# Kernel tuning notes

Hardware: AMD Instinct MI355X
Metric: run time of the kernel (lower is better)

The kernel has to match this reference:

```python
import jax, jax.numpy as jnp
import numpy as np

B, T, N, D = 64, 12, 207, 128
H, ORDER = 8, 2
HID = 2 * D  # mlp_ratio = 2


def _ln(x, g, b, eps=1e-5):
    m = x.mean(-1, keepdims=True)
    v = ((x - m) ** 2).mean(-1, keepdims=True)
    return (x - m) * jax.lax.rsqrt(v + eps) * g + b


def _l2norm(t, eps=1e-12):
    # matches torch.nn.functional.normalize(dim=-1)
    n = jnp.sqrt((t * t).sum(-1, keepdims=True))
    return t / jnp.maximum(n, eps)


def _fast_attn(q, k, v):
    # q, k, v: (B2, L, H, Dh); Performer-style linear attention from FastAttentionLayer.fast_attention
    q = _l2norm(q)
    k = _l2norm(k)
    L = q.shape[1]
    kvs = jnp.einsum('blhm,blhd->bhmd', k, v)
    num = jnp.einsum('bnhm,bhmd->bnhd', q, kvs) + L * v
    ks_sum = k.sum(axis=1)  # (B2, H, Dh)
    den = jnp.einsum('bnhm,bhm->bnh', q, ks_sum)[..., None] + L
    return num / jnp.maximum(den, 1e-5)


def _fast_layer(x, qkv_w, out_w, out_b):
    # x: (B, T, N, D). qkv_bias=False (mask arg), kernel=3 -> out_proj: Linear(2D, D)
    b, t, n, d = x.shape
    dh = d // H
    qkv = x @ qkv_w.T  # (B, T, N, 3D)
    q, k, v = jnp.split(qkv, 3, axis=-1)
    # spatial pass: attend over the N nodes for each (b, t)
    out_s = _fast_attn(q.reshape(b * t, n, H, dh),
                       k.reshape(b * t, n, H, dh),
                       v.reshape(b * t, n, H, dh)).reshape(b, t, n, d)
    # temporal pass: attend over the T steps for each (b, n)
    qt = q.transpose(0, 2, 1, 3).reshape(b * n, t, H, dh)
    kt = k.transpose(0, 2, 1, 3).reshape(b * n, t, H, dh)
    vt = v.transpose(0, 2, 1, 3).reshape(b * n, t, H, dh)
    out_t = _fast_attn(qt, kt, vt).reshape(b, n, t, d).transpose(0, 2, 1, 3)
    return jnp.concatenate([out_s, out_t], -1) @ out_w.T + out_b


def _forward(x, graph, qkv_w, out_w, out_b, pw_w, pw_b,
             fc1_w, fc1_b, fc2_w, fc2_b, ln1_g, ln1_b, ln2_g, ln2_b):
    # GraphPropagate: x_list = [x, graph @ x, ...] (Ks = ORDER hops)
    xs = [x]
    xk = x
    for _ in range(ORDER - 1):
        xk = jnp.einsum('thi,btij->bthj', graph, xk)
        xs.append(xk)
    # per-hop fast attention + zero-init pointwise branch, summed over hops
    agg = jnp.zeros_like(x)
    for i in range(ORDER):
        agg = agg + _fast_layer(xs[i], qkv_w[i], out_w[i], out_b[i]) + xs[i] @ pw_w[i].T + pw_b[i]
    h = _ln(x + agg, ln1_g, ln1_b)
    ff = jax.nn.relu(h @ fc1_w.T + fc1_b) @ fc2_w.T + fc2_b
    return _ln(h + ff, ln2_g, ln2_b)


def setup_inputs() -> dict:
    key = jax.random.key(0)
    ks = jax.random.split(key, 8)
    s = 0.02
    return {
        'x': jax.random.normal(ks[0], (B, T, N, D), jnp.float32),
        'graph': jax.random.uniform(ks[1], (T, N, N), jnp.float32) / N,
        'qkv_w': jax.random.normal(ks[2], (ORDER, 3 * D, D), jnp.float32) * s,
        'out_w': jax.random.normal(ks[3], (ORDER, D, 2 * D), jnp.float32) * s,
        'out_b': jnp.zeros((ORDER, D), jnp.float32),
        'pw_w': jax.random.normal(ks[4], (ORDER, D, D), jnp.float32) * s,
        'pw_b': jnp.zeros((ORDER, D), jnp.float32),
        'fc1_w': jax.random.normal(ks[5], (HID, D), jnp.float32) * s,
        'fc1_b': jnp.zeros((HID,), jnp.float32),
        'fc2_w': jax.random.normal(ks[6], (D, HID), jnp.float32) * s,
        'fc2_b': jnp.zeros((D,), jnp.float32),
        'ln1_g': jnp.ones((D,), jnp.float32),
        'ln1_b': jnp.zeros((D,), jnp.float32),
        'ln2_g': jnp.ones((D,), jnp.float32),
        'ln2_b': jnp.zeros((D,), jnp.float32),
    }


def reference(x, graph, qkv_w, out_w, out_b, pw_w, pw_b,
              fc1_w, fc1_b, fc2_w, fc2_b, ln1_g, ln1_b, ln2_g, ln2_b):
    return _forward(x, graph, qkv_w, out_w, out_b, pw_w, pw_b,
                    fc1_w, fc1_b, fc2_w, fc2_b, ln1_g, ln1_b, ln2_g, ln2_b)
```

## Files before the change

kernel.cpp:

```cpp
#include <hip/hip_runtime.h>
#include <hip/hip_bf16.h>

#define BB 64
#define TT 12
#define NN 207
#define DD 128
#define HH 8
#define DH 16
#define MROWS (BB*TT*NN)
#define KPAD 224
#define AW 768
#define CHB 32
#define CROWS (CHB*TT*NN)

typedef __bf16 bf16x8 __attribute__((ext_vector_type(8)));
typedef float  f32x4  __attribute__((ext_vector_type(4)));

__device__ inline float  b2f(__bf16 v){ return (float)v; }
__device__ inline __bf16 f2b(float v){ return (__bf16)v; }
__device__ inline bf16x8 ldfrag(const __bf16* p){ return *reinterpret_cast<const bf16x8*>(p); }

__device__ inline void gload_lds16(const __bf16* g, __bf16* l){
    __builtin_amdgcn_global_load_lds(
        (const __attribute__((address_space(1))) void*)(g),
        (__attribute__((address_space(3))) void*)(l), 16, 0, 0);
}
__device__ inline int swz(int r){ return (r ^ (r>>2)) & 3; }

__global__ __launch_bounds__(256) void xcopy_kernel(const float* __restrict__ x, __bf16* __restrict__ abuf)
{
    int nt = gridDim.x*256;
    for (int gIdx = blockIdx.x*256 + threadIdx.x; gIdx < MROWS*16; gIdx += nt) {
        int row = gIdx >> 4, c8 = (gIdx & 15)*8;
        const float* s = x + (size_t)row*DD + c8;
        f32x4 a = *reinterpret_cast<const f32x4*>(s);
        f32x4 b = *reinterpret_cast<const f32x4*>(s+4);
        bf16x8 r;
        #pragma unroll
        for (int i=0;i<4;i++){ r[i] = f2b(a[i]); r[i+4] = f2b(b[i]); }
        *reinterpret_cast<bf16x8*>(abuf + (size_t)row*AW + c8) = r;
    }
}

__global__ __launch_bounds__(256) void prep_misc_kernel(
    const float* __restrict__ graph, const float* __restrict__ qkv_w,
    const float* __restrict__ out_w, const float* __restrict__ out_b,
    const float* __restrict__ pw_w,  const float* __restrict__ pw_b,
    const float* __restrict__ fc1_w, const float* __restrict__ fc2_w,
    __bf16* __restrict__ gpad, __bf16* __restrict__ qkv_wb, __bf16* __restrict__ wcomb,
    __bf16* __restrict__ fc1_wb, __bf16* __restrict__ fc2_wb, float* __restrict__ bias_comb)
{
    int nt = gridDim.x*256;
    int tid = blockIdx.x*256 + threadIdx.x;
    for (int i = tid; i < TT*NN*KPAD; i += nt) {
        int k = i % KPAD, r = i / KPAD;
        gpad[i] = (k < NN) ? f2b(graph[(size_t)r*NN + k]) : f2b(0.f);
    }
    for (int i = tid; i < 2*3*DD*DD; i += nt) qkv_wb[i] = f2b(qkv_w[i]);
    for (int i = tid; i < DD*AW; i += nt) {
        int c = i / AW, j = i % AW;
        float v;
        if      (j < 128) v = pw_w[c*128 + j];
        else if (j < 256) v = pw_w[128*128 + c*128 + (j-128)];
        else if (j < 512) v = out_w[c*256 + (j-256)];
        else              v = out_w[128*256 + c*256 + (j-512)];
        wcomb[i] = f2b(v);
    }
    for (int i = tid; i < 2*DD*DD; i += nt) fc1_wb[i] = f2b(fc1_w[i]);
    for (int i = tid; i < 2*DD*DD; i += nt) fc2_wb[i] = f2b(fc2_w[i]);
    for (int i = tid; i < DD; i += nt)
        bias_comb[i] = pw_b[i] + pw_b[128+i] + out_b[i] + out_b[128+i];
}

__global__ __launch_bounds__(256) void propagate_kernel(const __bf16* __restrict__ gp,
    __bf16* __restrict__ abuf)
{
    int bt   = blockIdx.x;
    int t    = bt % TT;
    int tile = blockIdx.y;
    int lane = threadIdx.x & 63, w = threadIdx.x >> 6;
    int lhi = lane >> 4, llo = lane & 15;
    __shared__ __attribute__((aligned(16))) __bf16 XT[DD][40];
    const __bf16* xbt  = abuf + (size_t)bt*NN*AW;
    const __bf16* grow = gp + (size_t)t*NN*KPAD;
    int rowbase = tile*64 + w*16;
    f32x4 acc[8];
    #pragma unroll
    for (int i=0;i<8;i++) acc[i] = (f32x4){0.f,0.f,0.f,0.f};
    int arow = rowbase + llo; if (arow > NN-1) arow = NN-1;
    for (int k0=0; k0<KPAD; k0+=32) {
        __syncthreads();
        for (int kl = (threadIdx.x>>7); kl < 32; kl += 2) {
            int kk = k0 + kl, c = threadIdx.x & 127;
            XT[c][kl] = (kk < NN) ? xbt[(size_t)kk*AW + c] : f2b(0.f);
        }
        __syncthreads();
        bf16x8 a = ldfrag(grow + (size_t)arow*KPAD + k0 + lhi*8);
        #pragma unroll
        for (int cf=0;cf<8;cf++){
            bf16x8 b = *reinterpret_cast<const bf16x8*>(&XT[cf*16+llo][lhi*8]);
            acc[cf] = __builtin_amdgcn_mfma_f32_16x16x32_bf16(a, b, acc[cf], 0,0,0);
        }
    }
    #pragma unroll
    for (int e=0;e<4;e++){
        int row = rowbase + lhi*4 + e;
        if (row < NN) {
            #pragma unroll
            for (int cf=0;cf<8;cf++)
                abuf[((size_t)bt*NN + row)*AW + DD + cf*16 + llo] = f2b(acc[cf][e]);
        }
    }
}

template<int MODE, bool RELU>
__global__ __launch_bounds__(512) void gemm_kernel(const __bf16* __restrict__ A, size_t lda,
    const __bf16* __restrict__ W, const float* __restrict__ bias,
    void* out, size_t ldc, int K, int mend,
    const __bf16* __restrict__ resid, size_t ldr,
    const float* __restrict__ lng, const float* __restrict__ lnb)
{
    __shared__ __attribute__((aligned(16))) __bf16 lds[3][12288];
    int w = threadIdx.x >> 6, lane = threadIdx.x & 63;
    int lhi = lane >> 4, llo = lane & 15;
    size_t row0 = (size_t)blockIdx.x*256;
    int col0 = blockIdx.y*128;
    int nt = K >> 5;

    int sA0 = (w*2+0)*64 + lane, sA1 = (w*2+1)*64 + lane, sW = w*64 + lane;
    int rA0 = sA0>>2, uA0 = sA0&3, rA1 = sA1>>2, uA1 = sA1&3, rW = sW>>2, uW = sW&3;
    long gr0 = (long)row0 + rA0; if (gr0 >= mend) gr0 = mend-1;
    long gr1 = (long)row0 + rA1; if (gr1 >= mend) gr1 = mend-1;
    const __bf16* gA0 = A + (size_t)gr0*lda + ((uA0 ^ swz(rA0))<<3);
    const __bf16* gA1 = A + (size_t)gr1*lda + ((uA1 ^ swz(rA1))<<3);
    const __bf16* gW  = W + (size_t)(col0 + rW)*K + ((uW ^ swz(rW))<<3);
    int slotA0 = (w*2+0)*512 + (sA0&63)*8;
    int slotA1 = (w*2+1)*512 + (sA1&63)*8;
    int slotW  = 8192 + w*512 + (sW&63)*8;
    __bf16* base0 = &lds[0][0];

    int aoff[2], woff[8];
    #pragma unroll
    for (int rt=0;rt<2;rt++){
        int rl = w*32 + rt*16 + llo;
        aoff[rt] = rl*32 + ((lhi ^ swz(rl))<<3);
    }
    #pragma unroll
    for (int cf=0;cf<8;cf++){
        int wr = cf*16 + llo;
        woff[cf] = 8192 + wr*32 + ((lhi ^ swz(wr))<<3);
    }

    f32x4 acc[2][8];
    #pragma unroll
    for (int i=0;i<2;i++)
        #pragma unroll
        for (int j=0;j<8;j++) acc[i][j] = (f32x4){0.f,0.f,0.f,0.f};

    #define STAGE(buf, tt) { int k0 = (tt)<<5; __bf16* Lw = base0 + (buf)*12288;           \
        gload_lds16(gA0 + k0, Lw + (w*2+0)*512);                                           \
        gload_lds16(gA1 + k0, Lw + (w*2+1)*512);                                           \
        gload_lds16(gW  + k0, Lw + 8192 + w*512); }

    STAGE(0,0); STAGE(1,1); STAGE(2,2);

    int cur = 0;
    for (int t = 0; t < nt; ++t) {
        if (t <= nt-3)      asm volatile("s_waitcnt vmcnt(6)" ::: "memory");
        else if (t == nt-2) asm volatile("s_waitcnt vmcnt(3)" ::: "memory");
        else                asm volatile("s_waitcnt vmcnt(0)" ::: "memory");
        __builtin_amdgcn_s_barrier();
        __builtin_amdgcn_sched_barrier(0);
        const __bf16* Lb = base0 + cur*12288;
        bf16x8 a[2], b[8];
        #pragma unroll
        for (int rt=0;rt<2;rt++) a[rt] = *reinterpret_cast<const bf16x8*>(&Lb[aoff[rt]]);
        #pragma unroll
        for (int cf=0;cf<8;cf++)  b[cf] = *reinterpret_cast<const bf16x8*>(&Lb[woff[cf]]);
        asm volatile("s_waitcnt lgkmcnt(0)" ::: "memory");
        __builtin_amdgcn_sched_barrier(0);
        __builtin_amdgcn_s_barrier();
        if (t+3 < nt) STAGE(cur, t+3);
        #pragma unroll
        for (int rt=0;rt<2;rt++)
            #pragma unroll
            for (int cf=0;cf<8;cf++)
                acc[rt][cf] = __builtin_amdgcn_mfma_f32_16x16x32_bf16(a[rt], b[cf], acc[rt][cf], 0,0,0);
        cur = (cur == 2) ? 0 : cur + 1;
    }
    #undef STAGE

    float bv[8];
    #pragma unroll
    for (int cf=0;cf<8;cf++) bv[cf] = bias ? bias[col0 + cf*16 + llo] : 0.f;

    if (MODE == 0) {
        #pragma unroll
        for (int rt=0;rt<2;rt++) {
            #pragma unroll
            for (int e=0;e<4;e++) {
                size_t row = row0 + (size_t)w*32 + rt*16 + lhi*4 + e;
                if ((long)row >= mend) continue;
                #pragma unroll
                for (int cf=0;cf<8;cf++) {
                    float v = acc[rt][cf][e] + bv[cf];
                    if (RELU) v = fmaxf(v, 0.f);
                    ((__bf16*)out)[row*ldc + col0 + cf*16 + llo] = f2b(v);
                }
            }
        }
    } else {
        float g8[8], b8[8];
        #pragma unroll
        for (int cf=0;cf<8;cf++){ int c = cf*16 + llo; g8[cf] = lng[c]; b8[cf] = lnb[c]; }
        #pragma unroll
        for (int rt=0;rt<2;rt++) {
            #pragma unroll
            for (int e=0;e<4;e++) {
                size_t row = row0 + (size_t)w*32 + rt*16 + lhi*4 + e;
                if ((long)row >= mend) continue;
                float vals[8], s = 0.f, ss = 0.f;
                #pragma unroll
                for (int cf=0;cf<8;cf++) {
                    int c = cf*16 + llo;
                    float r = b2f(resid[row*ldr + c]);
                    float v = acc[rt][cf][e] + bv[cf] + r;
                    vals[cf] = v; s += v; ss += v*v;
                }
                #pragma unroll
                for (int o=1;o<16;o<<=1){ s += __shfl_xor(s,o,64); ss += __shfl_xor(ss,o,64); }
                float mean = s * (1.f/DD);
                float var  = ss * (1.f/DD) - mean*mean;
                float rs   = rsqrtf(var + 1e-5f);
                #pragma unroll
                for (int cf=0;cf<8;cf++) {
                    float v = (vals[cf]-mean)*rs*g8[cf] + b8[cf];
                    size_t idx = row*ldc + cf*16 + llo;
                    if (MODE == 3) ((__bf16*)out)[idx] = f2b(v);
                    else           ((float*)out)[idx]  = v;
                }
            }
        }
    }
}

#define CH 32
__global__ __launch_bounds__(256) void attn_s_kernel(const __bf16* __restrict__ qkv,
                                                     __bf16* __restrict__ outp)
{
    int bt = blockIdx.x;
    const __bf16* base = qkv + (size_t)bt*NN*384;
    __shared__ __attribute__((aligned(16))) __bf16 rows[CH][392];
    __shared__ float invq[224][8];
    __shared__ float invk_c[CH][8];
    __shared__ float ksum_l[8][16];
    int tid = threadIdx.x;
    int dd = tid & 15, half = (tid >> 4) & 1, h = tid >> 5;
    float kvs_col[16]; float ks = 0.f;
    #pragma unroll
    for (int m=0;m<16;m++) kvs_col[m] = 0.f;

    for (int c0 = 0; c0 < NN; c0 += CH) {
        __syncthreads();
        for (int i = tid; i < CH*48; i += 256) {
            int r = i/48, g = i%48; int n = c0 + r;
            bf16x8 v8 = (bf16x8){};
            if (n < NN) v8 = *reinterpret_cast<const bf16x8*>(base + (size_t)n*384 + g*8);
            *reinterpret_cast<bf16x8*>(&rows[r][g*8]) = v8;
        }
        __syncthreads();
        {
            int r = tid >> 3, hh = tid & 7;
            bf16x8 q0 = *reinterpret_cast<const bf16x8*>(&rows[r][hh*16]);
            bf16x8 q1 = *reinterpret_cast<const bf16x8*>(&rows[r][hh*16+8]);
            bf16x8 k0 = *reinterpret_cast<const bf16x8*>(&rows[r][128+hh*16]);
            bf16x8 k1 = *reinterpret_cast<const bf16x8*>(&rows[r][128+hh*16+8]);
            float sq = 0.f, sk = 0.f;
            #pragma unroll
            for (int m=0;m<8;m++){
                float a0=b2f(q0[m]), a1=b2f(q1[m]); sq += a0*a0 + a1*a1;
                float c0v=b2f(k0[m]), c1=b2f(k1[m]); sk += c0v*c0v + c1*c1;
            }
            invq[c0+r][hh] = 1.f/fmaxf(sqrtf(sq), 1e-12f);
            invk_c[r][hh]  = 1.f/fmaxf(sqrtf(sk), 1e-12f);
        }
        __syncthreads();
        #pragma unroll
        for (int i=0;i<CH/2;i++){
            int r = half*(CH/2) + i;
            float iv = invk_c[r][h];
            bf16x8 k0 = *reinterpret_cast<const bf16x8*>(&rows[r][128+h*16]);
            bf16x8 k1 = *reinterpret_cast<const bf16x8*>(&rows[r][128+h*16+8]);
            float vv  = b2f(rows[r][256+h*16+dd]);
            float kdd = b2f(rows[r][128+h*16+dd]);
            float t2 = iv*vv;
            #pragma unroll
            for (int m=0;m<8;m++){
                kvs_col[m]   += b2f(k0[m])*t2;
                kvs_col[m+8] += b2f(k1[m])*t2;
            }
            ks += kdd*iv;
        }
    }
    #pragma unroll
    for (int m=0;m<16;m++) kvs_col[m] += __shfl_xor(kvs_col[m], 16, 64);
    ks += __shfl_xor(ks, 16, 64);
    ksum_l[h][dd] = ks;
    __syncthreads();
    float ksr[16];
    #pragma unroll
    for (int m=0;m<16;m++) ksr[m] = ksum_l[h][m];

    for (int c0 = 0; c0 < NN; c0 += CH) {
        __syncthreads();
        for (int i = tid; i < CH*48; i += 256) {
            int r = i/48, g = i%48; int n = c0 + r;
            bf16x8 v8 = (bf16x8){};
            if (n < NN) v8 = *reinterpret_cast<const bf16x8*>(base + (size_t)n*384 + g*8);
            *reinterpret_cast<bf16x8*>(&rows[r][g*8]) = v8;
        }
        __syncthreads();
        #pragma unroll
        for (int i=0;i<CH/2;i++){
            int r = half*(CH/2) + i; int n = c0 + r;
            if (n >= NN) continue;
            float iq = invq[n][h];
            bf16x8 q0 = *reinterpret_cast<const bf16x8*>(&rows[r][h*16]);
            bf16x8 q1 = *reinterpret_cast<const bf16x8*>(&rows[r][h*16+8]);
            float num = 0.f, den = 0.f;
            #pragma unroll
            for (int m=0;m<8;m++){
                float qm0 = b2f(q0[m]), qm1 = b2f(q1[m]);
                num += qm0*kvs_col[m] + qm1*kvs_col[m+8];
                den += qm0*ksr[m]     + qm1*ksr[m+8];
            }
            float vv = b2f(rows[r][256+h*16+dd]);
            float o = (num*iq + (float)NN*vv) / fmaxf(den*iq + (float)NN, 1e-5f);
            outp[((size_t)bt*NN + n)*AW + h*16 + dd] = f2b(o);
        }
    }
}

__global__ __launch_bounds__(256) void attn_t_kernel(const __bf16* __restrict__ qkv,
                                                     __bf16* __restrict__ outp)
{
    int b = blockIdx.x;
    int nn0 = blockIdx.y * 2;
    __shared__ __attribute__((aligned(16))) __bf16 rows[TT][2][384];
    __shared__ float invq[2][TT][8], invk2[2][TT][8];
    int tid = threadIdx.x;
    for (int i = tid; i < TT*2*48; i += 256) {
        int t = i / 96, rem = i % 96;
        int nl = rem / 48, g = rem % 48;
        int nn = nn0 + nl;
        bf16x8 v8 = (bf16x8){};
        if (nn < NN) v8 = *reinterpret_cast<const bf16x8*>(qkv + ((size_t)(b*TT+t)*NN + nn)*384 + g*8);
        *reinterpret_cast<bf16x8*>(&rows[t][nl][g*8]) = v8;
    }
    __syncthreads();
    if (tid < 192) {
        int hh = tid & 7, t = (tid >> 3) % TT, nl = tid / 96;
        bf16x8 q0 = *reinterpret_cast<const bf16x8*>(&rows[t][nl][hh*16]);
        bf16x8 q1 = *reinterpret_cast<const bf16x8*>(&rows[t][nl][hh*16+8]);
        bf16x8 k0 = *reinterpret_cast<const bf16x8*>(&rows[t][nl][128+hh*16]);
        bf16x8 k1 = *reinterpret_cast<const bf16x8*>(&rows[t][nl][128+hh*16+8]);
        float sq = 0.f, sk = 0.f;
        #pragma unroll
        for (int m=0;m<8;m++){
            float a0=b2f(q0[m]), a1=b2f(q1[m]); sq += a0*a0 + a1*a1;
            float c0v=b2f(k0[m]), c1=b2f(k1[m]); sk += c0v*c0v + c1*c1;
        }
        invq[nl][t][hh]  = 1.f/fmaxf(sqrtf(sq), 1e-12f);
        invk2[nl][t][hh] = 1.f/fmaxf(sqrtf(sk), 1e-12f);
    }
    __syncthreads();
    int dd = tid & 15, h = (tid >> 4) & 7, nl = tid >> 7;
    int nn = nn0 + nl;
    float kvs_col[16], ksum[16];
    #pragma unroll
    for (int m=0;m<16;m++){ kvs_col[m]=0.f; ksum[m]=0.f; }
    #pragma unroll
    for (int t=0;t<TT;t++){
        float iv = invk2[nl][t][h];
        bf16x8 k0 = *reinterpret_cast<const bf16x8*>(&rows[t][nl][128+h*16]);
        bf16x8 k1 = *reinterpret_cast<const bf16x8*>(&rows[t][nl][128+h*16+8]);
        float vv = b2f(rows[t][nl][256+h*16+dd]);
        float t2 = iv*vv;
        #pragma unroll
        for (int m=0;m<8;m++){
            float km0 = b2f(k0[m]), km1 = b2f(k1[m]);
            kvs_col[m]   += km0*t2;  ksum[m]   += km0*iv;
            kvs_col[m+8] += km1*t2;  ksum[m+8] += km1*iv;
        }
    }
    #pragma unroll
    for (int t=0;t<TT;t++){
        float iq = invq[nl][t][h];
        bf16x8 q0 = *reinterpret_cast<const bf16x8*>(&rows[t][nl][h*16]);
        bf16x8 q1 = *reinterpret_cast<const bf16x8*>(&rows[t][nl][h*16+8]);
        float num = 0.f, den = 0.f;
        #pragma unroll
        for (int m=0;m<8;m++){
            float qm0 = b2f(q0[m]), qm1 = b2f(q1[m]);
            num += qm0*kvs_col[m]  + qm1*kvs_col[m+8];
            den += qm0*ksum[m]     + qm1*ksum[m+8];
        }
        float vv = b2f(rows[t][nl][256+h*16+dd]);
        float o = (num*iq + (float)TT*vv) / fmaxf(den*iq + (float)TT, 1e-5f);
        if (nn < NN)
            outp[((size_t)(b*TT+t)*NN + nn)*AW + h*16 + dd] = f2b(o);
    }
}

extern "C" void kernel_launch(void* const* d_in, const int* in_sizes, int n_in,
                              void* d_out, int out_size, void* d_ws, size_t ws_size,
                              hipStream_t stream)
{
    const float* x     = (const float*)d_in[0];
    const float* graph = (const float*)d_in[1];
    const float* qkv_w = (const float*)d_in[2];
    const float* out_w = (const float*)d_in[3];
    const float* out_b = (const float*)d_in[4];
    const float* pw_w  = (const float*)d_in[5];
    const float* pw_b  = (const float*)d_in[6];
    const float* fc1_w = (const float*)d_in[7];
    const float* fc1_b = (const float*)d_in[8];
    const float* fc2_w = (const float*)d_in[9];
    const float* fc2_b = (const float*)d_in[10];
    const float* ln1g  = (const float*)d_in[11];
    const float* ln1b  = (const float*)d_in[12];
    const float* ln2g  = (const float*)d_in[13];
    const float* ln2b  = (const float*)d_in[14];
    (void)in_sizes; (void)n_in; (void)out_size; (void)ws_size;

    char* ws = (char*)d_ws;
    size_t off = 0;
    __bf16* abuf = (__bf16*)(ws + off); off += (size_t)MROWS*AW*2;
    __bf16* qkvc = (__bf16*)(ws + off); off += (size_t)CROWS*3*DD*2;
    __bf16* gpad = (__bf16*)(ws + off); off += (size_t)TT*NN*KPAD*2;
    __bf16* qkv_wb = (__bf16*)(ws + off); off += (size_t)2*3*DD*DD*2;
    __bf16* wcomb  = (__bf16*)(ws + off); off += (size_t)DD*AW*2;
    __bf16* fc1_wb = (__bf16*)(ws + off); off += (size_t)2*DD*DD*2;
    __bf16* fc2_wb = (__bf16*)(ws + off); off += (size_t)2*DD*DD*2;
    float*  bias_comb = (float*)(ws + off); off += DD*4;

    dim3 blk(256), blk512(512);

    xcopy_kernel<<<dim3(4096), blk, 0, stream>>>(x, abuf);
    prep_misc_kernel<<<dim3(1024), blk, 0, stream>>>(graph, qkv_w, out_w, out_b, pw_w, pw_b,
        fc1_w, fc2_w, gpad, qkv_wb, wcomb, fc1_wb, fc2_wb, bias_comb);
    propagate_kernel<<<dim3(BB*TT, 4), blk, 0, stream>>>(gpad, abuf);

    for (int hop = 0; hop < 2; ++hop) {
        for (int c = 0; c < BB/CHB; ++c) {
            size_t rowoff = (size_t)c*CROWS;
            gemm_kernel<0,false><<<dim3((CROWS+255)/256, 3), blk512, 0, stream>>>(
                abuf + rowoff*AW + hop*DD, (size_t)AW, qkv_wb + (size_t)hop*3*DD*DD, nullptr,
                (void*)qkvc, (size_t)(3*DD), DD, CROWS, nullptr, 0, nullptr, nullptr);
            attn_s_kernel<<<dim3(CHB*TT), blk, 0, stream>>>(
                qkvc, abuf + rowoff*AW + 256 + hop*256);
            attn_t_kernel<<<dim3(CHB, (NN+1)/2), blk, 0, stream>>>(
                qkvc, abuf + rowoff*AW + 384 + hop*256);
        }
    }

    gemm_kernel<3,false><<<dim3(MROWS/256, 1), blk512, 0, stream>>>(
        abuf, (size_t)AW, wcomb, bias_comb, (void*)abuf, (size_t)AW, AW, MROWS,
        abuf, (size_t)AW, ln1g, ln1b);
    gemm_kernel<0,true><<<dim3(MROWS/256, 2), blk512, 0, stream>>>(
        abuf, (size_t)AW, fc1_wb, fc1_b, (void*)(abuf + 256), (size_t)AW, DD, MROWS,
        nullptr, 0, nullptr, nullptr);
    gemm_kernel<4,false><<<dim3(MROWS/256, 1), blk512, 0, stream>>>(
        abuf + 256, (size_t)AW, fc2_wb, fc2_b, d_out, (size_t)DD, 2*DD, MROWS,
        abuf, (size_t)AW, ln2g, ln2b);
}
```

Baseline: 837.9 us.

## Retile GEMM to 128x128 blocks with 2x2 wave layout and LDS LayerNorm reduction

The GEMM block tile shrinks from 256x128 with 512 threads to 128x128 with 256 threads. Each wave now computes a 64x64 sub-tile arranged 2x2, instead of 32x128 strips. This gives more register reuse per fragment load and, with launch_bounds(256,3), more blocks per CU. Because a row is now split across two waves, the fused LayerNorm epilogue combines partial sums and squared sums through LDS with a block barrier. It also reloads the residual instead of keeping values in registers, which adds extra global reads. The CROWS/128 grid relies on the row count dividing evenly.

```diff
diff --git a/kernel.cpp b/kernel.cpp
--- a/kernel.cpp
+++ b/kernel.cpp
@@ -114,130 +114,149 @@
 }
 
 template<int MODE, bool RELU>
-__global__ __launch_bounds__(512) void gemm_kernel(const __bf16* __restrict__ A, size_t lda,
+__global__ __launch_bounds__(256, 3) void gemm_kernel(const __bf16* __restrict__ A, size_t lda,
     const __bf16* __restrict__ W, const float* __restrict__ bias,
     void* out, size_t ldc, int K, int mend,
     const __bf16* __restrict__ resid, size_t ldr,
     const float* __restrict__ lng, const float* __restrict__ lnb)
 {
-    __shared__ __attribute__((aligned(16))) __bf16 lds[3][12288];
+    __shared__ __attribute__((aligned(16))) __bf16 lds[3][8192];
     int w = threadIdx.x >> 6, lane = threadIdx.x & 63;
     int lhi = lane >> 4, llo = lane & 15;
-    size_t row0 = (size_t)blockIdx.x*256;
+    int wr = w >> 1, wc = w & 1;
+    size_t row0 = (size_t)blockIdx.x*128;
     int col0 = blockIdx.y*128;
     int nt = K >> 5;
 
-    int sA0 = (w*2+0)*64 + lane, sA1 = (w*2+1)*64 + lane, sW = w*64 + lane;
-    int rA0 = sA0>>2, uA0 = sA0&3, rA1 = sA1>>2, uA1 = sA1&3, rW = sW>>2, uW = sW&3;
-    long gr0 = (long)row0 + rA0; if (gr0 >= mend) gr0 = mend-1;
-    long gr1 = (long)row0 + rA1; if (gr1 >= mend) gr1 = mend-1;
-    const __bf16* gA0 = A + (size_t)gr0*lda + ((uA0 ^ swz(rA0))<<3);
-    const __bf16* gA1 = A + (size_t)gr1*lda + ((uA1 ^ swz(rA1))<<3);
-    const __bf16* gW  = W + (size_t)(col0 + rW)*K + ((uW ^ swz(rW))<<3);
-    int slotA0 = (w*2+0)*512 + (sA0&63)*8;
-    int slotA1 = (w*2+1)*512 + (sA1&63)*8;
-    int slotW  = 8192 + w*512 + (sW&63)*8;
-    __bf16* base0 = &lds[0][0];
-
-    int aoff[2], woff[8];
-    #pragma unroll
-    for (int rt=0;rt<2;rt++){
-        int rl = w*32 + rt*16 + llo;
+    const __bf16* gA[2]; const __bf16* gW[2];
+    #pragma unroll
+    for (int j=0;j<2;j++){
+        int rl = j*16 + (lane>>2);
+        int u  = lane & 3;
+        int rA = w*32 + rl;
+        long gr = (long)row0 + rA; if (gr >= mend) gr = mend-1;
+        gA[j] = A + (size_t)gr*lda + ((u ^ swz(rA))<<3);
+        gW[j] = W + (size_t)(col0 + rA)*K + ((u ^ swz(rA))<<3);
+    }
+
+    int aoff[4], woff[4];
+    #pragma unroll
+    for (int rt=0;rt<4;rt++){
+        int rl = wr*64 + rt*16 + llo;
         aoff[rt] = rl*32 + ((lhi ^ swz(rl))<<3);
     }
     #pragma unroll
-    for (int cf=0;cf<8;cf++){
-        int wr = cf*16 + llo;
-        woff[cf] = 8192 + wr*32 + ((lhi ^ swz(wr))<<3);
-    }
-
-    f32x4 acc[2][8];
-    #pragma unroll
-    for (int i=0;i<2;i++)
-        #pragma unroll
-        for (int j=0;j<8;j++) acc[i][j] = (f32x4){0.f,0.f,0.f,0.f};
-
-    #define STAGE(buf, tt) { int k0 = (tt)<<5; __bf16* Lw = base0 + (buf)*12288;           \
-        gload_lds16(gA0 + k0, Lw + (w*2+0)*512);                                           \
-        gload_lds16(gA1 + k0, Lw + (w*2+1)*512);                                           \
-        gload_lds16(gW  + k0, Lw + 8192 + w*512); }
+    for (int cf=0;cf<4;cf++){
+        int wrow = wc*64 + cf*16 + llo;
+        woff[cf] = 4096 + wrow*32 + ((lhi ^ swz(wrow))<<3);
+    }
+
+    f32x4 acc[4][4];
+    #pragma unroll
+    for (int i=0;i<4;i++)
+        #pragma unroll
+        for (int j=0;j<4;j++) acc[i][j] = (f32x4){0.f,0.f,0.f,0.f};
+
+    #define STAGE(buf, tt) { int k0 = (tt)<<5; __bf16* L = &lds[buf][0];   \
+        gload_lds16(gA[0] + k0, L + w*1024);                               \
+        gload_lds16(gA[1] + k0, L + w*1024 + 512);                         \
+        gload_lds16(gW[0] + k0, L + 4096 + w*1024);                        \
+        gload_lds16(gW[1] + k0, L + 4096 + w*1024 + 512); }
 
     STAGE(0,0); STAGE(1,1); STAGE(2,2);
 
     int cur = 0;
     for (int t = 0; t < nt; ++t) {
-        if (t <= nt-3)      asm volatile("s_waitcnt vmcnt(6)" ::: "memory");
-        else if (t == nt-2) asm volatile("s_waitcnt vmcnt(3)" ::: "memory");
+        if (t < nt-2)       asm volatile("s_waitcnt vmcnt(8)" ::: "memory");
+        else if (t == nt-2) asm volatile("s_waitcnt vmcnt(4)" ::: "memory");
         else                asm volatile("s_waitcnt vmcnt(0)" ::: "memory");
         __builtin_amdgcn_s_barrier();
         __builtin_amdgcn_sched_barrier(0);
-        const __bf16* Lb = base0 + cur*12288;
-        bf16x8 a[2], b[8];
-        #pragma unroll
-        for (int rt=0;rt<2;rt++) a[rt] = *reinterpret_cast<const bf16x8*>(&Lb[aoff[rt]]);
-        #pragma unroll
-        for (int cf=0;cf<8;cf++)  b[cf] = *reinterpret_cast<const bf16x8*>(&Lb[woff[cf]]);
+        const __bf16* Lb = &lds[cur][0];
+        bf16x8 a[4], b[4];
+        #pragma unroll
+        for (int rt=0;rt<4;rt++) a[rt] = *reinterpret_cast<const bf16x8*>(&Lb[aoff[rt]]);
+        #pragma unroll
+        for (int cf=0;cf<4;cf++)  b[cf] = *reinterpret_cast<const bf16x8*>(&Lb[woff[cf]]);
         asm volatile("s_waitcnt lgkmcnt(0)" ::: "memory");
         __builtin_amdgcn_sched_barrier(0);
         __builtin_amdgcn_s_barrier();
         if (t+3 < nt) STAGE(cur, t+3);
         #pragma unroll
-        for (int rt=0;rt<2;rt++)
-            #pragma unroll
-            for (int cf=0;cf<8;cf++)
+        for (int rt=0;rt<4;rt++)
+            #pragma unroll
+            for (int cf=0;cf<4;cf++)
                 acc[rt][cf] = __builtin_amdgcn_mfma_f32_16x16x32_bf16(a[rt], b[cf], acc[rt][cf], 0,0,0);
         cur = (cur == 2) ? 0 : cur + 1;
     }
     #undef STAGE
 
-    float bv[8];
-    #pragma unroll
-    for (int cf=0;cf<8;cf++) bv[cf] = bias ? bias[col0 + cf*16 + llo] : 0.f;
+    float bv[4];
+    #pragma unroll
+    for (int cf=0;cf<4;cf++) bv[cf] = bias ? bias[col0 + wc*64 + cf*16 + llo] : 0.f;
 
     if (MODE == 0) {
         #pragma unroll
-        for (int rt=0;rt<2;rt++) {
+        for (int rt=0;rt<4;rt++) {
             #pragma unroll
             for (int e=0;e<4;e++) {
-                size_t row = row0 + (size_t)w*32 + rt*16 + lhi*4 + e;
+                size_t row = row0 + (size_t)wr*64 + rt*16 + lhi*4 + e;
                 if ((long)row >= mend) continue;
                 #pragma unroll
-                for (int cf=0;cf<8;cf++) {
+                for (int cf=0;cf<4;cf++) {
                     float v = acc[rt][cf][e] + bv[cf];
                     if (RELU) v = fmaxf(v, 0.f);
-                    ((__bf16*)out)[row*ldc + col0 + cf*16 + llo] = f2b(v);
+                    ((__bf16*)out)[row*ldc + col0 + wc*64 + cf*16 + llo] = f2b(v);
                 }
             }
         }
     } else {
-        float g8[8], b8[8];
-        #pragma unroll
-        for (int cf=0;cf<8;cf++){ int c = cf*16 + llo; g8[cf] = lng[c]; b8[cf] = lnb[c]; }
-        #pragma unroll
-        for (int rt=0;rt<2;rt++) {
+        float g4[4], b4[4];
+        #pragma unroll
+        for (int cf=0;cf<4;cf++){ int c = wc*64 + cf*16 + llo; g4[cf] = lng[c]; b4[cf] = lnb[c]; }
+        float* fl = (float*)&lds[0][0];
+        #pragma unroll
+        for (int rt=0;rt<4;rt++) {
             #pragma unroll
             for (int e=0;e<4;e++) {
-                size_t row = row0 + (size_t)w*32 + rt*16 + lhi*4 + e;
+                int rowl = wr*64 + rt*16 + lhi*4 + e;
+                size_t row = row0 + rowl;
                 if ((long)row >= mend) continue;
-                float vals[8], s = 0.f, ss = 0.f;
+                float s = 0.f, ss = 0.f;
                 #pragma unroll
-                for (int cf=0;cf<8;cf++) {
-                    int c = cf*16 + llo;
+                for (int cf=0;cf<4;cf++) {
+                    int c = wc*64 + cf*16 + llo;
                     float r = b2f(resid[row*ldr + c]);
                     float v = acc[rt][cf][e] + bv[cf] + r;
-                    vals[cf] = v; s += v; ss += v*v;
+                    s += v; ss += v*v;
                 }
                 #pragma unroll
                 for (int o=1;o<16;o<<=1){ s += __shfl_xor(s,o,64); ss += __shfl_xor(ss,o,64); }
+                if (llo == 0) { fl[rowl*4 + wc*2] = s; fl[rowl*4 + wc*2 + 1] = ss; }
+            }
+        }
+        __syncthreads();
+        #pragma unroll
+        for (int rt=0;rt<4;rt++) {
+            #pragma unroll
+            for (int e=0;e<4;e++) {
+                int rowl = wr*64 + rt*16 + lhi*4 + e;
+                size_t row = row0 + rowl;
+                if ((long)row >= mend) continue;
+                float s  = fl[rowl*4]   + fl[rowl*4+2];
+                float ss = fl[rowl*4+1] + fl[rowl*4+3];
                 float mean = s * (1.f/DD);
                 float var  = ss * (1.f/DD) - mean*mean;
                 float rs   = rsqrtf(var + 1e-5f);
                 #pragma unroll
-                for (int cf=0;cf<8;cf++) {
-                    float v = (vals[cf]-mean)*rs*g8[cf] + b8[cf];
-                    size_t idx = row*ldc + cf*16 + llo;
-                    if (MODE == 3) ((__bf16*)out)[idx] = f2b(v);
-                    else           ((float*)out)[idx]  = v;
+                for (int cf=0;cf<4;cf++) {
+                    int c = wc*64 + cf*16 + llo;
+                    float r = b2f(resid[row*ldr + c]);
+                    float v = acc[rt][cf][e] + bv[cf] + r;
+                    float o = (v-mean)*rs*g4[cf] + b4[cf];
+                    size_t idx = row*ldc + c;
+                    if (MODE == 3) ((__bf16*)out)[idx] = f2b(o);
+                    else           ((float*)out)[idx]  = o;
                 }
             }
         }
@@ -444,7 +463,7 @@
     __bf16* fc2_wb = (__bf16*)(ws + off); off += (size_t)2*DD*DD*2;
     float*  bias_comb = (float*)(ws + off); off += DD*4;
 
-    dim3 blk(256), blk512(512);
+    dim3 blk(256);
 
     xcopy_kernel<<<dim3(4096), blk, 0, stream>>>(x, abuf);
     prep_misc_kernel<<<dim3(1024), blk, 0, stream>>>(graph, qkv_w, out_w, out_b, pw_w, pw_b,
@@ -454,7 +473,7 @@
     for (int hop = 0; hop < 2; ++hop) {
         for (int c = 0; c < BB/CHB; ++c) {
             size_t rowoff = (size_t)c*CROWS;
-            gemm_kernel<0,false><<<dim3((CROWS+255)/256, 3), blk512, 0, stream>>>(
+            gemm_kernel<0,false><<<dim3(CROWS/128, 3), blk, 0, stream>>>(
                 abuf + rowoff*AW + hop*DD, (size_t)AW, qkv_wb + (size_t)hop*3*DD*DD, nullptr,
                 (void*)qkvc, (size_t)(3*DD), DD, CROWS, nullptr, 0, nullptr, nullptr);
             attn_s_kernel<<<dim3(CHB*TT), blk, 0, stream>>>(
@@ -464,13 +483,13 @@
         }
     }
 
-    gemm_kernel<3,false><<<dim3(MROWS/256, 1), blk512, 0, stream>>>(
+    gemm_kernel<3,false><<<dim3(MROWS/128, 1), blk, 0, stream>>>(
         abuf, (size_t)AW, wcomb, bias_comb, (void*)abuf, (size_t)AW, AW, MROWS,
         abuf, (size_t)AW, ln1g, ln1b);
-    gemm_kernel<0,true><<<dim3(MROWS/256, 2), blk512, 0, stream>>>(
+    gemm_kernel<0,true><<<dim3(MROWS/128, 2), blk, 0, stream>>>(
         abuf, (size_t)AW, fc1_wb, fc1_b, (void*)(abuf + 256), (size_t)AW, DD, MROWS,
         nullptr, 0, nullptr, nullptr);
-    gemm_kernel<4,false><<<dim3(MROWS/256, 1), blk512, 0, stream>>>(
+    gemm_kernel<4,false><<<dim3(MROWS/128, 1), blk, 0, stream>>>(
         abuf + 256, (size_t)AW, fc2_wb, fc2_b, d_out, (size_t)DD, 2*DD, MROWS,
         abuf, (size_t)AW, ln2g, ln2b);
 }
```

Result: slower. 883.5 us (+5.4%).

## Add persistent K=128 GEMM with register-resident weights; cache Q/V in spatial attention

Applied to the files above, without the earlier changes.

Adds a persistent sgemm_k128 kernel for the K=128 GEMMs (QKV projection and fc1). It keeps the weight fragments in registers and streams 16-row A tiles through a triple-buffered LDS pipeline using direct global-to-LDS loads and explicit vmcnt waits. The spatial attention kernel now keeps Q and V for all nodes in LDS during the first pass, so the second pass over qkv global memory and its syncs go away. This raises register and LDS pressure, which may reduce occupancy.

```diff
diff --git a/kernel.cpp b/kernel.cpp
--- a/kernel.cpp
+++ b/kernel.cpp
@@ -14,6 +14,7 @@
 #define CROWS (CHB*TT*NN)
 
 typedef __bf16 bf16x8 __attribute__((ext_vector_type(8)));
+typedef __bf16 bf16x4 __attribute__((ext_vector_type(4)));
 typedef float  f32x4  __attribute__((ext_vector_type(4)));
 
 __device__ inline float  b2f(__bf16 v){ return (float)v; }
@@ -134,9 +135,6 @@
     const __bf16* gA0 = A + (size_t)gr0*lda + ((uA0 ^ swz(rA0))<<3);
     const __bf16* gA1 = A + (size_t)gr1*lda + ((uA1 ^ swz(rA1))<<3);
     const __bf16* gW  = W + (size_t)(col0 + rW)*K + ((uW ^ swz(rW))<<3);
-    int slotA0 = (w*2+0)*512 + (sA0&63)*8;
-    int slotA1 = (w*2+1)*512 + (sA1&63)*8;
-    int slotW  = 8192 + w*512 + (sW&63)*8;
     __bf16* base0 = &lds[0][0];
 
     int aoff[2], woff[8];
@@ -244,13 +242,104 @@
     }
 }
 
+template<bool RELU>
+__global__ __launch_bounds__(256) void sgemm_k128(const __bf16* __restrict__ A, size_t lda,
+    const __bf16* __restrict__ W, const float* __restrict__ bias,
+    __bf16* __restrict__ out, size_t ldc, int ngroups)
+{
+    __shared__ __attribute__((aligned(16))) __bf16 lds[12][2048];
+    int w = threadIdx.x >> 6, lane = threadIdx.x & 63;
+    int lhi = lane >> 4, llo = lane & 15;
+    int col0 = blockIdx.y*128;
+
+    bf16x8 wf[4][8];
+    #pragma unroll
+    for (int ks=0;ks<4;ks++)
+        #pragma unroll
+        for (int cf=0;cf<8;cf++)
+            wf[ks][cf] = ldfrag(W + (size_t)(col0 + cf*16 + llo)*128 + ks*32 + lhi*8);
+
+    f32x4 bvv[8];
+    #pragma unroll
+    for (int cf=0;cf<8;cf++){
+        if (bias) bvv[cf] = *reinterpret_cast<const f32x4*>(bias + col0 + cf*16 + lhi*4);
+        else      bvv[cf] = (f32x4){0.f,0.f,0.f,0.f};
+    }
+
+    size_t gsrc[4];
+    #pragma unroll
+    for (int j=0;j<4;j++){
+        int r = j*4 + lhi;
+        int u = llo ^ r;
+        gsrc[j] = (size_t)r*lda + (size_t)u*8;
+    }
+    int aoff[4];
+    #pragma unroll
+    for (int ks=0;ks<4;ks++) aoff[ks] = llo*128 + (((ks<<2)|lhi) ^ llo)*8;
+
+    int gw = blockIdx.x*4 + w, stride = gridDim.x*4;
+    int n = (gw < ngroups) ? ((ngroups-1-gw)/stride + 1) : 0;
+    __bf16* slab0 = &lds[w*3][0];
+
+    #define SSTAGE(i) { size_t rbase = (size_t)(gw + (size_t)(i)*stride)*16*lda;           \
+        __bf16* L = slab0 + ((i)%3)*2048;                                                  \
+        gload_lds16(A + rbase + gsrc[0], L);                                               \
+        gload_lds16(A + rbase + gsrc[1], L + 512);                                         \
+        gload_lds16(A + rbase + gsrc[2], L + 1024);                                        \
+        gload_lds16(A + rbase + gsrc[3], L + 1536); }
+
+    if (n > 0) SSTAGE(0);
+    if (n > 1) SSTAGE(1);
+
+    for (int i = 0; i < n; ++i) {
+        int kept = ((i+1 < n) ? 4 : 0) + ((i >= 2) ? 16 : i*8);
+        if      (kept >= 20) asm volatile("s_waitcnt vmcnt(20)" ::: "memory");
+        else if (kept == 16) asm volatile("s_waitcnt vmcnt(16)" ::: "memory");
+        else if (kept == 12) asm volatile("s_waitcnt vmcnt(12)" ::: "memory");
+        else if (kept == 8)  asm volatile("s_waitcnt vmcnt(8)"  ::: "memory");
+        else if (kept == 4)  asm volatile("s_waitcnt vmcnt(4)"  ::: "memory");
+        else                 asm volatile("s_waitcnt vmcnt(0)"  ::: "memory");
+
+        const __bf16* Ls = slab0 + (i%3)*2048;
+        bf16x8 a[4];
+        #pragma unroll
+        for (int ks=0;ks<4;ks++) a[ks] = *reinterpret_cast<const bf16x8*>(&Ls[aoff[ks]]);
+
+        if (i+2 < n) SSTAGE(i+2);
+
+        f32x4 acc[8];
+        #pragma unroll
+        for (int cf=0;cf<8;cf++) acc[cf] = (f32x4){0.f,0.f,0.f,0.f};
+        #pragma unroll
+        for (int ks=0;ks<4;ks++)
+            #pragma unroll
+            for (int cf=0;cf<8;cf++)
+                acc[cf] = __builtin_amdgcn_mfma_f32_16x16x32_bf16(wf[ks][cf], a[ks], acc[cf], 0,0,0);
+
+        size_t grow = (size_t)(gw + (size_t)i*stride)*16 + llo;
+        #pragma unroll
+        for (int cf=0;cf<8;cf++){
+            bf16x4 o;
+            #pragma unroll
+            for (int e=0;e<4;e++){
+                float v = acc[cf][e] + bvv[cf][e];
+                if (RELU) v = fmaxf(v, 0.f);
+                o[e] = f2b(v);
+            }
+            *reinterpret_cast<bf16x4*>(out + grow*ldc + col0 + cf*16 + lhi*4) = o;
+        }
+    }
+    #undef SSTAGE
+}
+
 #define CH 32
 __global__ __launch_bounds__(256) void attn_s_kernel(const __bf16* __restrict__ qkv,
                                                      __bf16* __restrict__ outp)
 {
     int bt = blockIdx.x;
     const __bf16* base = qkv + (size_t)bt*NN*384;
-    __shared__ __attribute__((aligned(16))) __bf16 rows[CH][392];
+    __shared__ __attribute__((aligned(16))) __bf16 qv[224][264];
+    __shared__ __attribute__((aligned(16))) __bf16 kbuf[CH][136];
     __shared__ float invq[224][8];
     __shared__ float invk_c[CH][8];
     __shared__ float ksum_l[8][16];
@@ -263,18 +352,20 @@
     for (int c0 = 0; c0 < NN; c0 += CH) {
         __syncthreads();
         for (int i = tid; i < CH*48; i += 256) {
-            int r = i/48, g = i%48; int n = c0 + r;
+            int r = i/48, g = i%48; int nn = c0 + r;
             bf16x8 v8 = (bf16x8){};
-            if (n < NN) v8 = *reinterpret_cast<const bf16x8*>(base + (size_t)n*384 + g*8);
-            *reinterpret_cast<bf16x8*>(&rows[r][g*8]) = v8;
+            if (nn < NN) v8 = *reinterpret_cast<const bf16x8*>(base + (size_t)nn*384 + g*8);
+            if (g < 16)      *reinterpret_cast<bf16x8*>(&qv[c0+r][g*8]) = v8;
+            else if (g < 32) *reinterpret_cast<bf16x8*>(&kbuf[r][(g-16)*8]) = v8;
+            else             *reinterpret_cast<bf16x8*>(&qv[c0+r][128 + (g-32)*8]) = v8;
         }
         __syncthreads();
         {
             int r = tid >> 3, hh = tid & 7;
-            bf16x8 q0 = *reinterpret_cast<const bf16x8*>(&rows[r][hh*16]);
-            bf16x8 q1 = *reinterpret_cast<const bf16x8*>(&rows[r][hh*16+8]);
-            bf16x8 k0 = *reinterpret_cast<const bf16x8*>(&rows[r][128+hh*16]);
-            bf16x8 k1 = *reinterpret_cast<const bf16x8*>(&rows[r][128+hh*16+8]);
+            bf16x8 q0 = *reinterpret_cast<const bf16x8*>(&qv[c0+r][hh*16]);
+            bf16x8 q1 = *reinterpret_cast<const bf16x8*>(&qv[c0+r][hh*16+8]);
+            bf16x8 k0 = *reinterpret_cast<const bf16x8*>(&kbuf[r][hh*16]);
+            bf16x8 k1 = *reinterpret_cast<const bf16x8*>(&kbuf[r][hh*16+8]);
             float sq = 0.f, sk = 0.f;
             #pragma unroll
             for (int m=0;m<8;m++){
@@ -289,10 +380,10 @@
         for (int i=0;i<CH/2;i++){
             int r = half*(CH/2) + i;
             float iv = invk_c[r][h];
-            bf16x8 k0 = *reinterpret_cast<const bf16x8*>(&rows[r][128+h*16]);
-            bf16x8 k1 = *reinterpret_cast<const bf16x8*>(&rows[r][128+h*16+8]);
-            float vv  = b2f(rows[r][256+h*16+dd]);
-            float kdd = b2f(rows[r][128+h*16+dd]);
+            bf16x8 k0 = *reinterpret_cast<const bf16x8*>(&kbuf[r][h*16]);
+            bf16x8 k1 = *reinterpret_cast<const bf16x8*>(&kbuf[r][h*16+8]);
+            float vv  = b2f(qv[c0+r][128+h*16+dd]);
+            float kdd = b2f(kbuf[r][h*16+dd]);
             float t2 = iv*vv;
             #pragma unroll
             for (int m=0;m<8;m++){
@@ -311,33 +402,20 @@
     #pragma unroll
     for (int m=0;m<16;m++) ksr[m] = ksum_l[h][m];
 
-    for (int c0 = 0; c0 < NN; c0 += CH) {
-        __syncthreads();
-        for (int i = tid; i < CH*48; i += 256) {
-            int r = i/48, g = i%48; int n = c0 + r;
-            bf16x8 v8 = (bf16x8){};
-            if (n < NN) v8 = *reinterpret_cast<const bf16x8*>(base + (size_t)n*384 + g*8);
-            *reinterpret_cast<bf16x8*>(&rows[r][g*8]) = v8;
-        }
-        __syncthreads();
-        #pragma unroll
-        for (int i=0;i<CH/2;i++){
-            int r = half*(CH/2) + i; int n = c0 + r;
-            if (n >= NN) continue;
-            float iq = invq[n][h];
-            bf16x8 q0 = *reinterpret_cast<const bf16x8*>(&rows[r][h*16]);
-            bf16x8 q1 = *reinterpret_cast<const bf16x8*>(&rows[r][h*16+8]);
-            float num = 0.f, den = 0.f;
-            #pragma unroll
-            for (int m=0;m<8;m++){
-                float qm0 = b2f(q0[m]), qm1 = b2f(q1[m]);
-                num += qm0*kvs_col[m] + qm1*kvs_col[m+8];
-                den += qm0*ksr[m]     + qm1*ksr[m+8];
-            }
-            float vv = b2f(rows[r][256+h*16+dd]);
-            float o = (num*iq + (float)NN*vv) / fmaxf(den*iq + (float)NN, 1e-5f);
-            outp[((size_t)bt*NN + n)*AW + h*16 + dd] = f2b(o);
-        }
+    for (int nn = half; nn < NN; nn += 2) {
+        float iq = invq[nn][h];
+        bf16x8 q0 = *reinterpret_cast<const bf16x8*>(&qv[nn][h*16]);
+        bf16x8 q1 = *reinterpret_cast<const bf16x8*>(&qv[nn][h*16+8]);
+        float num = 0.f, den = 0.f;
+        #pragma unroll
+        for (int m=0;m<8;m++){
+            float qm0 = b2f(q0[m]), qm1 = b2f(q1[m]);
+            num += qm0*kvs_col[m] + qm1*kvs_col[m+8];
+            den += qm0*ksr[m]     + qm1*ksr[m+8];
+        }
+        float vv = b2f(qv[nn][128+h*16+dd]);
+        float o = (num*iq + (float)NN*vv) / fmaxf(den*iq + (float)NN, 1e-5f);
+        outp[((size_t)bt*NN + nn)*AW + h*16 + dd] = f2b(o);
     }
 }
 
@@ -454,9 +532,9 @@
     for (int hop = 0; hop < 2; ++hop) {
         for (int c = 0; c < BB/CHB; ++c) {
             size_t rowoff = (size_t)c*CROWS;
-            gemm_kernel<0,false><<<dim3((CROWS+255)/256, 3), blk512, 0, stream>>>(
+            sgemm_k128<false><<<dim3(170, 3), blk, 0, stream>>>(
                 abuf + rowoff*AW + hop*DD, (size_t)AW, qkv_wb + (size_t)hop*3*DD*DD, nullptr,
-                (void*)qkvc, (size_t)(3*DD), DD, CROWS, nullptr, 0, nullptr, nullptr);
+                qkvc, (size_t)(3*DD), CROWS/16);
             attn_s_kernel<<<dim3(CHB*TT), blk, 0, stream>>>(
                 qkvc, abuf + rowoff*AW + 256 + hop*256);
             attn_t_kernel<<<dim3(CHB, (NN+1)/2), blk, 0, stream>>>(
@@ -467,9 +545,8 @@
     gemm_kernel<3,false><<<dim3(MROWS/256, 1), blk512, 0, stream>>>(
         abuf, (size_t)AW, wcomb, bias_comb, (void*)abuf, (size_t)AW, AW, MROWS,
         abuf, (size_t)AW, ln1g, ln1b);
-    gemm_kernel<0,true><<<dim3(MROWS/256, 2), blk512, 0, stream>>>(
-        abuf, (size_t)AW, fc1_wb, fc1_b, (void*)(abuf + 256), (size_t)AW, DD, MROWS,
-        nullptr, 0, nullptr, nullptr);
+    sgemm_k128<true><<<dim3(256, 2), blk, 0, stream>>>(
+        abuf, (size_t)AW, fc1_wb, fc1_b, abuf + 256, (size_t)AW, MROWS/16);
     gemm_kernel<4,false><<<dim3(MROWS/256, 1), blk512, 0, stream>>>(
         abuf + 256, (size_t)AW, fc2_wb, fc2_b, d_out, (size_t)DD, 2*DD, MROWS,
         abuf, (size_t)AW, ln2g, ln2b);
```

After: 988.7 us. +18.0%, slower.
